# Optimization experiments

Hardware: AMD Instinct MI355X
Metric: run time of the kernel (lower is better)

Reference implementation:

```python
import jax, jax.numpy as jnp
import numpy as np

D = 1024
H = 16
DH = D // H  # 64
EPS = 1e-6


def setup_inputs() -> dict:
    key = jax.random.key(0)
    ks = jax.random.split(key, 12)
    B, Nq, Nk = 4, 2048, 2048
    s = 1.0 / np.sqrt(D)
    return {
        "x": jax.random.normal(ks[0], (B, Nq, D), dtype=jnp.float32),
        "context": jax.random.normal(ks[1], (B, Nk, D), dtype=jnp.float32),
        "Wq": jax.random.normal(ks[2], (D, D), dtype=jnp.float32) * s,
        "bq": jnp.zeros((D,), dtype=jnp.float32),
        "Wk": jax.random.normal(ks[3], (D, D), dtype=jnp.float32) * s,
        "bk": jnp.zeros((D,), dtype=jnp.float32),
        "Wv": jax.random.normal(ks[4], (D, D), dtype=jnp.float32) * s,
        "bv": jnp.zeros((D,), dtype=jnp.float32),
        "Wo": jax.random.normal(ks[5], (D, D), dtype=jnp.float32) * s,
        "bo": jnp.zeros((D,), dtype=jnp.float32),
    }


def _split_heads(t):
    B, N, _ = t.shape
    return t.reshape(B, N, H, DH).transpose(0, 2, 1, 3)  # (B,H,N,DH)


def reference(x, context, Wq, bq, Wk, bk, Wv, bv, Wo, bo):
    B, Nq, _ = x.shape
    # QKV projections (torch Linear: x @ W.T + b)
    q = _split_heads(x @ Wq.T + bq)          # (B,H,Nq,DH)
    k = _split_heads(context @ Wk.T + bk)    # (B,H,Nk,DH)
    v = _split_heads(context @ Wv.T + bv)    # (B,H,Nk,DH)
    # QK-norm (use_qk_norm=True), scale buffer = 1.0
    q = q / (jnp.linalg.norm(q, axis=-1, keepdims=True) + EPS)
    k = k / (jnp.linalg.norm(k, axis=-1, keepdims=True) + EPS)
    scale = jnp.float32(1.0)
    attn = jnp.einsum("bhqd,bhkd->bhqk", q, k) * scale
    attn = jax.nn.softmax(attn, axis=-1)
    out = jnp.einsum("bhqk,bhkd->bhqd", attn, v)  # (B,H,Nq,DH)
    out = out.transpose(0, 2, 1, 3).reshape(B, Nq, D)
    return out @ Wo.T + bo
```

## Files before the change

kernel.cpp:

```cpp
#include <hip/hip_runtime.h>

typedef unsigned short u16;
typedef unsigned int u32;
typedef __attribute__((ext_vector_type(8))) short bf16x8;
typedef __attribute__((ext_vector_type(4))) float f32x4;
typedef __attribute__((ext_vector_type(16))) float f32x16;
typedef __attribute__((ext_vector_type(4))) u32 u32x4;

#define D_MODEL 1024
#define NHEAD 16
#define DHEAD 64
#define SEQ 2048
#define BATCH 4
#define MTOT (BATCH * SEQ)
#define LOG2E 1.4426950408889634f

#define MFMA16(A, B, C) __builtin_amdgcn_mfma_f32_16x16x32_bf16((A), (B), (C), 0, 0, 0)
#define MFMA32(A, B, C) __builtin_amdgcn_mfma_f32_32x32x16_bf16((A), (B), (C), 0, 0, 0)

__device__ __forceinline__ u16 f2bf(float f) {
  u32 u = __builtin_bit_cast(u32, f);
  u = (u + 0x7FFFu + ((u >> 16) & 1u)) >> 16;
  return (u16)u;
}

__device__ __forceinline__ void async_copy16(void* lds, const void* g) {
  __builtin_amdgcn_global_load_lds(
      (const __attribute__((address_space(1))) u32*)g,
      (__attribute__((address_space(3))) u32*)lds, 16, 0, 0);
}

__device__ __forceinline__ u32 cvtpk_bf16(float lo, float hi) {
  u32 r;
  asm("v_cvt_pk_bf16_f32 %0, %1, %2" : "=v"(r) : "v"(lo), "v"(hi));
  return r;
}
__device__ __forceinline__ void permswap(u32& a, u32& b) {
  asm("v_permlane32_swap_b32 %0, %1" : "+v"(a), "+v"(b));
}

__global__ void cvt2(const float* __restrict__ s0, u16* __restrict__ d0,
                     const float* __restrict__ s1, u16* __restrict__ d1, int n4) {
  int i = blockIdx.x * blockDim.x + threadIdx.x;
  int st = gridDim.x * blockDim.x;
  for (; i < 2 * n4; i += st) {
    const float* s = (i < n4) ? s0 : s1;
    u16* d = (i < n4) ? d0 : d1;
    int j = (i < n4) ? i : (i - n4);
    float4 v = ((const float4*)s)[j];
    ushort4 o;
    o.x = f2bf(v.x); o.y = f2bf(v.y); o.z = f2bf(v.z); o.w = f2bf(v.w);
    ((ushort4*)d)[j] = o;
  }
}

#define BM 128
#define BN 128
#define BKG 64

template <int SM>
__global__ __launch_bounds__(256, 2) void gemm_bt(const u16* __restrict__ A,
                                                  const u16* __restrict__ Bw,
                                                  const float* __restrict__ bias,
                                                  void* __restrict__ Cout,
                                                  int M, int N, int K, float sMul) {
  __shared__ u16 As[BM * BKG];
  __shared__ u16 Bs[BN * BKG];
  const int tid = threadIdx.x;
  const int l = tid & 63;
  const int wid = tid >> 6;
  const int nwg = gridDim.x;
  const int bid = blockIdx.x;
  const int cpx = nwg >> 3;
  const int swz = (bid & 7) * cpx + (bid >> 3);
  const int ntile = N / BN;
  const int m0 = (swz / ntile) * BM;
  const int n0 = (swz % ntile) * BN;
  const int wr = wid >> 1, wc = wid & 1;
  const int r = l & 15, kg = l >> 4;
  f32x4 acc[4][4] = {};
  char* AsB = (char*)As;
  char* BsB = (char*)Bs;
  const int arow = l >> 3;
  const int agran = (l & 7) ^ arow;

  for (int kt = 0; kt < K; kt += BKG) {
#pragma unroll
    for (int cc = 0; cc < 4; ++cc) {
      int c = wid + (cc << 2);
      int rowi = (c << 3) + arow;
      const char* ga = (const char*)A + ((size_t)(m0 + rowi) * K + kt) * 2 + agran * 16;
      async_copy16(AsB + c * 1024, ga);
      const char* gb = (const char*)Bw + ((size_t)(n0 + rowi) * K + kt) * 2 + agran * 16;
      async_copy16(BsB + c * 1024, gb);
    }
    __syncthreads();
#pragma unroll
    for (int half = 0; half < 2; ++half) {
      const int g = ((half << 2) + kg) ^ (r & 7);
      bf16x8 af[4], bf[4];
#pragma unroll
      for (int i = 0; i < 4; ++i) {
        af[i] = *(const bf16x8*)(AsB + (wr * 64 + i * 16 + r) * 128 + g * 16);
        bf[i] = *(const bf16x8*)(BsB + (wc * 64 + i * 16 + r) * 128 + g * 16);
      }
#pragma unroll
      for (int i = 0; i < 4; ++i)
#pragma unroll
        for (int j = 0; j < 4; ++j)
          acc[i][j] = MFMA16(af[i], bf[j], acc[i][j]);
    }
    __syncthreads();
  }

  if (SM == 3) {
    u16* C = (u16*)Cout;
    float bvj[4];
#pragma unroll
    for (int j = 0; j < 4; ++j) bvj[j] = bias[n0 + wc * 64 + j * 16 + r];
#pragma unroll
    for (int i = 0; i < 4; ++i) {
      const int row0 = m0 + wr * 64 + i * 16 + kg * 4;
#pragma unroll
      for (int jj = 0; jj < 4; ++jj) {
        float t[4];
        float s2 = 0.f;
#pragma unroll
        for (int j = 0; j < 4; ++j) {
          t[j] = acc[i][j][jj] + bvj[j];
          s2 += t[j] * t[j];
        }
        s2 += __shfl_xor(s2, 1);
        s2 += __shfl_xor(s2, 2);
        s2 += __shfl_xor(s2, 4);
        s2 += __shfl_xor(s2, 8);
        const float inv = sMul / (sqrtf(s2) + 1e-6f);
#pragma unroll
        for (int j = 0; j < 4; ++j)
          C[(size_t)(row0 + jj) * N + n0 + wc * 64 + j * 16 + r] = f2bf(t[j] * inv);
      }
    }
    return;
  }

#pragma unroll
  for (int i = 0; i < 4; ++i) {
#pragma unroll
    for (int j = 0; j < 4; ++j) {
      const int col = n0 + wc * 64 + j * 16 + r;
      const float bv = bias[col];
      const int row0 = m0 + wr * 64 + i * 16 + kg * 4;
      if (SM == 1) {
        float* C = (float*)Cout;
#pragma unroll
        for (int jj = 0; jj < 4; ++jj)
          C[(size_t)(row0 + jj) * N + col] = acc[i][j][jj] + bv;
      } else {
        u16* C = (u16*)Cout;
        const int hh = col >> 6, dh = col & 63;
        const int bb = row0 >> 11, tok = row0 & 2047;
        ushort4 o;
        o.x = f2bf(acc[i][j][0] + bv);
        o.y = f2bf(acc[i][j][1] + bv);
        o.z = f2bf(acc[i][j][2] + bv);
        o.w = f2bf(acc[i][j][3] + bv);
        *(ushort4*)(C + ((size_t)((bb * 16 + hh) * 64 + dh) * SEQ + tok)) = o;
      }
    }
  }
}

#define KVB 64
#define NT (SEQ / KVB)

__global__ __launch_bounds__(256, 4) void attn_kernel(const u16* __restrict__ Q,
                                                      const u16* __restrict__ K,
                                                      const u16* __restrict__ Vt,
                                                      u16* __restrict__ O) {
  __shared__ alignas(16) u16 Ks[2][KVB * 64];
  __shared__ alignas(16) u16 Vs[2][64 * KVB];
  const int tid = threadIdx.x;
  const int l = tid & 63;
  const int wid = tid >> 6;
  const int qg = l & 31;
  const int half = l >> 5;
  const int bid = blockIdx.x;
  const int swz = (bid & 7) * 128 + (bid >> 3);
  const int qt = swz & 15;
  const int bh = swz >> 4;
  const int b = bh >> 4, h = bh & 15;

  const int srow = l >> 3, slot = l & 7;
  const int r0 = (wid << 3) + srow;
  const int r1 = ((wid + 4) << 3) + srow;
  const int sw0 = (r0 ^ (r0 >> 3)) & 7;
  const int sw1 = (r1 ^ (r1 >> 3)) & 7;
  const u16* pK0 = K + ((size_t)(b * SEQ) + r0) * D_MODEL + h * 64 + (slot ^ sw0) * 8;
  const u16* pK1 = K + ((size_t)(b * SEQ) + r1) * D_MODEL + h * 64 + (slot ^ sw1) * 8;
  const u16* pV0 = Vt + ((size_t)(bh * 64) + r0) * SEQ + (slot ^ sw0) * 8;
  const u16* pV1 = Vt + ((size_t)(bh * 64) + r1) * SEQ + (slot ^ sw1) * 8;
  const int ldsc0 = wid * 1024, ldsc1 = (wid + 4) * 1024;

  bf16x8 qf[4];
  {
    const u16* q0 = Q + ((size_t)(b * SEQ + qt * 128 + wid * 32 + qg)) * D_MODEL + h * 64 + half * 8;
#pragma unroll
    for (int dc = 0; dc < 4; ++dc) qf[dc] = *(const bf16x8*)(q0 + dc * 16);
  }
  f32x16 oacc[2] = {};
  float lrun = 0.f;

  auto stage = [&](int bufi) {
    char* KsX = (char*)Ks[bufi];
    char* VsX = (char*)Vs[bufi];
    async_copy16(KsX + ldsc0, pK0);
    async_copy16(KsX + ldsc1, pK1);
    async_copy16(VsX + ldsc0, pV0);
    async_copy16(VsX + ldsc1, pV1);
    pK0 += (size_t)KVB * D_MODEL;
    pK1 += (size_t)KVB * D_MODEL;
    pV0 += KVB;
    pV1 += KVB;
  };

  stage(0);
  __syncthreads();
  int buf = 0;

  for (int t = 0; t < NT; ++t) {
    if (t + 1 < NT) stage(buf ^ 1);
    const char* KsC = (const char*)Ks[buf];
    const char* VsC = (const char*)Vs[buf];

    f32x16 st[2] = {};
    __builtin_amdgcn_s_setprio(1);
#pragma unroll
    for (int t32 = 0; t32 < 2; ++t32) {
      const int rowK = t32 * 32 + qg;
      const int swk = (rowK ^ (rowK >> 3)) & 7;
#pragma unroll
      for (int dc = 0; dc < 4; ++dc) {
        const int p = (dc * 2 + half) ^ swk;
        bf16x8 kf = *(const bf16x8*)(KsC + rowK * 128 + p * 16);
        st[t32] = MFMA32(kf, qf[dc], st[t32]);
      }
    }
    __builtin_amdgcn_s_setprio(0);

    float rs0 = 0.f, rs1 = 0.f, rs2 = 0.f, rs3 = 0.f;
#pragma unroll
    for (int t32 = 0; t32 < 2; ++t32)
#pragma unroll
      for (int rr = 0; rr < 16; rr += 4) {
        float p0 = __builtin_amdgcn_exp2f(st[t32][rr + 0]);
        float p1 = __builtin_amdgcn_exp2f(st[t32][rr + 1]);
        float p2 = __builtin_amdgcn_exp2f(st[t32][rr + 2]);
        float p3 = __builtin_amdgcn_exp2f(st[t32][rr + 3]);
        st[t32][rr + 0] = p0; st[t32][rr + 1] = p1;
        st[t32][rr + 2] = p2; st[t32][rr + 3] = p3;
        rs0 += p0; rs1 += p1; rs2 += p2; rs3 += p3;
      }
    lrun += (rs0 + rs1) + (rs2 + rs3);

#pragma unroll
    for (int t32 = 0; t32 < 2; ++t32) {
#pragma unroll
      for (int cc = 0; cc < 2; ++cc) {
        const int base = cc * 8;
        u32 wA = cvtpk_bf16(st[t32][base + 0], st[t32][base + 1]);
        u32 wB = cvtpk_bf16(st[t32][base + 2], st[t32][base + 3]);
        u32 wC = cvtpk_bf16(st[t32][base + 4], st[t32][base + 5]);
        u32 wD = cvtpk_bf16(st[t32][base + 6], st[t32][base + 7]);
        permswap(wA, wC);
        permswap(wB, wD);
        u32x4 pw = {wA, wB, wC, wD};
        bf16x8 pf = __builtin_bit_cast(bf16x8, pw);
        const int qw = ((t32 * 2 + cc) << 1) + half;
        __builtin_amdgcn_s_setprio(1);
#pragma unroll
        for (int dt = 0; dt < 2; ++dt) {
          const int rowV = dt * 32 + qg;
          const int pp = qw ^ ((rowV ^ (rowV >> 3)) & 7);
          bf16x8 vf = *(const bf16x8*)(VsC + rowV * 128 + pp * 16);
          oacc[dt] = MFMA32(vf, pf, oacc[dt]);
        }
        __builtin_amdgcn_s_setprio(0);
      }
    }
    __syncthreads();
    buf ^= 1;
  }

  lrun += __shfl_xor(lrun, 32);
  const float inv = 1.0f / lrun;
  u32* orow = (u32*)(O + ((size_t)(b * SEQ + qt * 128 + wid * 32 + qg)) * D_MODEL + h * 64);
#pragma unroll
  for (int dt = 0; dt < 2; ++dt)
#pragma unroll
    for (int w = 0; w < 8; ++w) {
      const int dh = dt * 32 + (w & 1) * 2 + 8 * (w >> 1) + 4 * half;
      u32 pk = cvtpk_bf16(oacc[dt][2 * w] * inv, oacc[dt][2 * w + 1] * inv);
      orow[dh >> 1] = pk;
    }
}

extern "C" void kernel_launch(void* const* d_in, const int* in_sizes, int n_in,
                              void* d_out, int out_size, void* d_ws, size_t ws_size,
                              hipStream_t stream) {
  const float* x   = (const float*)d_in[0];
  const float* ctx = (const float*)d_in[1];
  const float* Wq  = (const float*)d_in[2];
  const float* bq  = (const float*)d_in[3];
  const float* Wk  = (const float*)d_in[4];
  const float* bk  = (const float*)d_in[5];
  const float* Wv  = (const float*)d_in[6];
  const float* bv  = (const float*)d_in[7];
  const float* Wo  = (const float*)d_in[8];
  const float* bo  = (const float*)d_in[9];
  float* out = (float*)d_out;

  const size_t NTOK = (size_t)MTOT * D_MODEL;
  const size_t WSZ = (size_t)D_MODEL * D_MODEL;
  u16* xb  = (u16*)d_ws;
  u16* cb  = xb + NTOK;
  u16* wqb = cb + NTOK;
  u16* wkb = wqb + WSZ;
  u16* wvb = wkb + WSZ;
  u16* wob = wvb + WSZ;
  u16* Qb  = wob + WSZ;
  u16* Kb  = Qb + NTOK;
  u16* Vtb = Kb + NTOK;
  (void)in_sizes; (void)n_in; (void)out_size; (void)ws_size;

  dim3 blk(256);
  cvt2<<<2048, blk, 0, stream>>>(x, xb, ctx, cb, (int)(NTOK / 4));
  cvt2<<<512, blk, 0, stream>>>(Wq, wqb, Wk, wkb, (int)(WSZ / 4));
  cvt2<<<512, blk, 0, stream>>>(Wv, wvb, Wo, wob, (int)(WSZ / 4));

  gemm_bt<3><<<512, blk, 0, stream>>>(xb, wqb, bq, Qb, MTOT, D_MODEL, D_MODEL, LOG2E);
  gemm_bt<3><<<512, blk, 0, stream>>>(cb, wkb, bk, Kb, MTOT, D_MODEL, D_MODEL, 1.0f);
  gemm_bt<2><<<512, blk, 0, stream>>>(cb, wvb, bv, Vtb, MTOT, D_MODEL, D_MODEL, 0.f);

  attn_kernel<<<1024, blk, 0, stream>>>(Qb, Kb, Vtb, xb);

  gemm_bt<1><<<512, blk, 0, stream>>>(xb, wob, bo, out, MTOT, D_MODEL, D_MODEL, 0.f);
}
```

Measured before the change: 197.7 us.

## Fuse Q/K/V projection GEMMs into one launch with concatenated KV weights

Replaces three separate projection GEMM launches with a single 1536-block kernel. Each block picks the Q or KV problem from its swizzled block id and reads Wk and Wv as one contiguous 2048-row weight (wkb followed by wvb). This removes launch gaps and tail underutilisation, and the occupancy hint goes from 2 to 3 blocks per CU. The attention kernel also seeds the first QK MFMA with an opaque zero vector instead of a zero-initialised accumulator, to avoid per-tile register zeroing; the output GEMM becomes a specialised non-template kernel.

```diff
diff --git a/kernel.cpp b/kernel.cpp
--- a/kernel.cpp
+++ b/kernel.cpp
@@ -54,28 +54,34 @@
   }
 }
 
-#define BM 128
-#define BN 128
-#define BKG 64
-
-template <int SM>
-__global__ __launch_bounds__(256, 2) void gemm_bt(const u16* __restrict__ A,
-                                                  const u16* __restrict__ Bw,
-                                                  const float* __restrict__ bias,
-                                                  void* __restrict__ Cout,
-                                                  int M, int N, int K, float sMul) {
-  __shared__ u16 As[BM * BKG];
-  __shared__ u16 Bs[BN * BKG];
+__global__ __launch_bounds__(256, 3) void gemm_qkv(
+    const u16* __restrict__ xb, const u16* __restrict__ cb,
+    const u16* __restrict__ wqb, const u16* __restrict__ wkvb,
+    const float* __restrict__ bq, const float* __restrict__ bk,
+    const float* __restrict__ bv,
+    u16* __restrict__ Qb, u16* __restrict__ Kb, u16* __restrict__ Vtb) {
+  __shared__ u16 As[128 * 64];
+  __shared__ u16 Bs[128 * 64];
+  const int K = 1024;
   const int tid = threadIdx.x;
   const int l = tid & 63;
   const int wid = tid >> 6;
-  const int nwg = gridDim.x;
   const int bid = blockIdx.x;
-  const int cpx = nwg >> 3;
-  const int swz = (bid & 7) * cpx + (bid >> 3);
-  const int ntile = N / BN;
-  const int m0 = (swz / ntile) * BM;
-  const int n0 = (swz % ntile) * BN;
+  const int swz = (bid & 7) * 192 + (bid >> 3);
+  const bool isQ = swz < 512;
+  const u16* A;
+  const u16* Bw;
+  int m0, n0;
+  if (isQ) {
+    A = xb; Bw = wqb;
+    m0 = (swz >> 3) * 128;
+    n0 = (swz & 7) * 128;
+  } else {
+    const int s = swz - 512;
+    A = cb; Bw = wkvb;
+    m0 = (s >> 4) * 128;
+    n0 = (s & 15) * 128;
+  }
   const int wr = wid >> 1, wc = wid & 1;
   const int r = l & 15, kg = l >> 4;
   f32x4 acc[4][4] = {};
@@ -84,7 +90,7 @@
   const int arow = l >> 3;
   const int agran = (l & 7) ^ arow;
 
-  for (int kt = 0; kt < K; kt += BKG) {
+  for (int kt = 0; kt < K; kt += 64) {
 #pragma unroll
     for (int cc = 0; cc < 4; ++cc) {
       int c = wid + (cc << 2);
@@ -113,11 +119,15 @@
     __syncthreads();
   }
 
-  if (SM == 3) {
-    u16* C = (u16*)Cout;
+  const int colbase = n0 + wc * 64;
+  const bool isV = (!isQ) && (colbase >= 1024);
+  if (!isV) {
+    u16* C = isQ ? Qb : Kb;
+    const float* bias = isQ ? bq : bk;
+    const float sMul = isQ ? LOG2E : 1.0f;
     float bvj[4];
 #pragma unroll
-    for (int j = 0; j < 4; ++j) bvj[j] = bias[n0 + wc * 64 + j * 16 + r];
+    for (int j = 0; j < 4; ++j) bvj[j] = bias[colbase + j * 16 + r];
 #pragma unroll
     for (int i = 0; i < 4; ++i) {
       const int row0 = m0 + wr * 64 + i * 16 + kg * 4;
@@ -137,35 +147,90 @@
         const float inv = sMul / (sqrtf(s2) + 1e-6f);
 #pragma unroll
         for (int j = 0; j < 4; ++j)
-          C[(size_t)(row0 + jj) * N + n0 + wc * 64 + j * 16 + r] = f2bf(t[j] * inv);
-      }
-    }
-    return;
-  }
-
+          C[(size_t)(row0 + jj) * D_MODEL + colbase + j * 16 + r] = f2bf(t[j] * inv);
+      }
+    }
+  } else {
+#pragma unroll
+    for (int i = 0; i < 4; ++i) {
+#pragma unroll
+      for (int j = 0; j < 4; ++j) {
+        const int col = colbase + j * 16 + r;
+        const float bvv = bv[col - 1024];
+        const int row0 = m0 + wr * 64 + i * 16 + kg * 4;
+        const int hh = (col - 1024) >> 6, dh = col & 63;
+        const int bb = row0 >> 11, tok = row0 & 2047;
+        ushort4 o;
+        o.x = f2bf(acc[i][j][0] + bvv);
+        o.y = f2bf(acc[i][j][1] + bvv);
+        o.z = f2bf(acc[i][j][2] + bvv);
+        o.w = f2bf(acc[i][j][3] + bvv);
+        *(ushort4*)(Vtb + ((size_t)((bb * 16 + hh) * 64 + dh) * SEQ + tok)) = o;
+      }
+    }
+  }
+}
+
+__global__ __launch_bounds__(256, 3) void gemm_out(const u16* __restrict__ A,
+                                                   const u16* __restrict__ Bw,
+                                                   const float* __restrict__ bias,
+                                                   float* __restrict__ Cout) {
+  __shared__ u16 As[128 * 64];
+  __shared__ u16 Bs[128 * 64];
+  const int K = 1024, N = 1024;
+  const int tid = threadIdx.x;
+  const int l = tid & 63;
+  const int wid = tid >> 6;
+  const int bid = blockIdx.x;
+  const int swz = (bid & 7) * 64 + (bid >> 3);
+  const int m0 = (swz >> 3) * 128;
+  const int n0 = (swz & 7) * 128;
+  const int wr = wid >> 1, wc = wid & 1;
+  const int r = l & 15, kg = l >> 4;
+  f32x4 acc[4][4] = {};
+  char* AsB = (char*)As;
+  char* BsB = (char*)Bs;
+  const int arow = l >> 3;
+  const int agran = (l & 7) ^ arow;
+
+  for (int kt = 0; kt < K; kt += 64) {
+#pragma unroll
+    for (int cc = 0; cc < 4; ++cc) {
+      int c = wid + (cc << 2);
+      int rowi = (c << 3) + arow;
+      const char* ga = (const char*)A + ((size_t)(m0 + rowi) * K + kt) * 2 + agran * 16;
+      async_copy16(AsB + c * 1024, ga);
+      const char* gb = (const char*)Bw + ((size_t)(n0 + rowi) * K + kt) * 2 + agran * 16;
+      async_copy16(BsB + c * 1024, gb);
+    }
+    __syncthreads();
+#pragma unroll
+    for (int half = 0; half < 2; ++half) {
+      const int g = ((half << 2) + kg) ^ (r & 7);
+      bf16x8 af[4], bf[4];
+#pragma unroll
+      for (int i = 0; i < 4; ++i) {
+        af[i] = *(const bf16x8*)(AsB + (wr * 64 + i * 16 + r) * 128 + g * 16);
+        bf[i] = *(const bf16x8*)(BsB + (wc * 64 + i * 16 + r) * 128 + g * 16);
+      }
+#pragma unroll
+      for (int i = 0; i < 4; ++i)
+#pragma unroll
+        for (int j = 0; j < 4; ++j)
+          acc[i][j] = MFMA16(af[i], bf[j], acc[i][j]);
+    }
+    __syncthreads();
+  }
 #pragma unroll
   for (int i = 0; i < 4; ++i) {
 #pragma unroll
     for (int j = 0; j < 4; ++j) {
       const int col = n0 + wc * 64 + j * 16 + r;
-      const float bv = bias[col];
+      const float bvv = bias[col];
       const int row0 = m0 + wr * 64 + i * 16 + kg * 4;
-      if (SM == 1) {
-        float* C = (float*)Cout;
-#pragma unroll
-        for (int jj = 0; jj < 4; ++jj)
-          C[(size_t)(row0 + jj) * N + col] = acc[i][j][jj] + bv;
-      } else {
-        u16* C = (u16*)Cout;
-        const int hh = col >> 6, dh = col & 63;
-        const int bb = row0 >> 11, tok = row0 & 2047;
-        ushort4 o;
-        o.x = f2bf(acc[i][j][0] + bv);
-        o.y = f2bf(acc[i][j][1] + bv);
-        o.z = f2bf(acc[i][j][2] + bv);
-        o.w = f2bf(acc[i][j][3] + bv);
-        *(ushort4*)(C + ((size_t)((bb * 16 + hh) * 64 + dh) * SEQ + tok)) = o;
-      }
+#pragma unroll
+      for (int jj = 0; jj < 4; ++jj)
+        Cout[(size_t)(row0 + jj) * N + col] = acc[i][j][jj] + bvv;
     }
   }
 }
@@ -207,6 +272,12 @@
 #pragma unroll
     for (int dc = 0; dc < 4; ++dc) qf[dc] = *(const bf16x8*)(q0 + dc * 16);
   }
+  float z0 = 0.f;
+  asm("" : "+v"(z0));
+  f32x16 zc;
+#pragma unroll
+  for (int i = 0; i < 16; ++i) zc[i] = z0;
+
   f32x16 oacc[2] = {};
   float lrun = 0.f;
 
@@ -232,14 +303,16 @@
     const char* KsC = (const char*)Ks[buf];
     const char* VsC = (const char*)Vs[buf];
 
-    f32x16 st[2] = {};
+    f32x16 st[2];
     __builtin_amdgcn_s_setprio(1);
 #pragma unroll
     for (int t32 = 0; t32 < 2; ++t32) {
       const int rowK = t32 * 32 + qg;
       const int swk = (rowK ^ (rowK >> 3)) & 7;
-#pragma unroll
-      for (int dc = 0; dc < 4; ++dc) {
+      bf16x8 kf0 = *(const bf16x8*)(KsC + rowK * 128 + (half ^ swk) * 16);
+      st[t32] = MFMA32(kf0, qf[0], zc);
+#pragma unroll
+      for (int dc = 1; dc < 4; ++dc) {
         const int p = (dc * 2 + half) ^ swk;
         bf16x8 kf = *(const bf16x8*)(KsC + rowK * 128 + p * 16);
         st[t32] = MFMA32(kf, qf[dc], st[t32]);
@@ -337,11 +410,9 @@
   cvt2<<<512, blk, 0, stream>>>(Wq, wqb, Wk, wkb, (int)(WSZ / 4));
   cvt2<<<512, blk, 0, stream>>>(Wv, wvb, Wo, wob, (int)(WSZ / 4));
 
-  gemm_bt<3><<<512, blk, 0, stream>>>(xb, wqb, bq, Qb, MTOT, D_MODEL, D_MODEL, LOG2E);
-  gemm_bt<3><<<512, blk, 0, stream>>>(cb, wkb, bk, Kb, MTOT, D_MODEL, D_MODEL, 1.0f);
-  gemm_bt<2><<<512, blk, 0, stream>>>(cb, wvb, bv, Vtb, MTOT, D_MODEL, D_MODEL, 0.f);
+  gemm_qkv<<<1536, blk, 0, stream>>>(xb, cb, wqb, wkb, bq, bk, bv, Qb, Kb, Vtb);
 
   attn_kernel<<<1024, blk, 0, stream>>>(Qb, Kb, Vtb, xb);
 
-  gemm_bt<1><<<512, blk, 0, stream>>>(xb, wob, bo, out, MTOT, D_MODEL, D_MODEL, 0.f);
-}
+  gemm_out<<<512, blk, 0, stream>>>(xb, wob, bo, out);
+}
```

Result: no change. 197.0 us (-0.3%).
